# Kernel optimization log

Hardware: AMD Instinct MI355X
Metric: run time of the kernel (lower is better)

## Reference

```python
import jax, jax.numpy as jnp
import numpy as np

N_NODES = 100000
N_EDGES = 600000
D_FEAT = 128


def setup_inputs() -> dict:
    key = jax.random.key(0)
    kx, kh, kt, kp = jax.random.split(key, 4)
    x = jax.random.normal(kx, (N_NODES, D_FEAT), dtype=jnp.float32)
    # ensure every node appears at least once as a source (h) so deg > 0
    base = jax.random.permutation(kp, jnp.arange(N_NODES, dtype=jnp.int64))
    extra = jax.random.randint(kh, (N_EDGES - N_NODES,), 0, N_NODES, dtype=jnp.int64)
    h = jnp.concatenate([base, extra])
    t = jax.random.randint(kt, (N_EDGES,), 0, N_NODES, dtype=jnp.int64)
    return {"x": x, "h": h, "t": t}


def reference(x, h, t):
    n = x.shape[0]
    # degree of source nodes h  (torch_geometric.utils.degree)
    deg = jnp.zeros((n,), dtype=x.dtype).at[h].add(jnp.asarray(1, x.dtype))
    deg_inv_sqrt = deg ** -0.5
    norm = deg_inv_sqrt[t] * deg_inv_sqrt[h]  # [E]
    # spmm with row=t, col=h: out[t] += norm * x[h]
    msgs = norm[:, None] * x[h]  # [E, D]
    out = jax.ops.segment_sum(msgs, t, num_segments=n)  # [N, D]
    return jax.nn.relu(out)
```

## Files before the change

kernel.cpp:

```cpp
#include <hip/hip_runtime.h>

#define D_FEAT 128
#define KB 16
#define CBINS 25600
#define CNR 4
#define NWIN 25
#define PBINS 12800
#define PNR 8
#define CBLK 1024
#define SCAN_BLK 1024

__device__ __forceinline__ unsigned short f2bf_rtn(float f) {
    unsigned int u = __float_as_uint(f);
    unsigned int r = (u + 0x7FFFu + ((u >> 16) & 1u)) >> 16;
    return (unsigned short)r;
}

__global__ void __launch_bounds__(CBLK) count_convert_kernel(
    const int* __restrict__ h, const int* __restrict__ t,
    unsigned* __restrict__ tmat, unsigned* __restrict__ hmat,
    int* __restrict__ wsums,
    const float* __restrict__ x, unsigned short* __restrict__ xb,
    int E, int slice4, int n4)
{
    __shared__ unsigned cnt[CBINS / 2];
    const int nt = CNR * KB;
    int bid = blockIdx.x;
    if (bid >= 2 * nt) {
        int idx = (bid - 2 * nt) * CBLK + threadIdx.x;
        if (idx < n4) {
            float4 v = reinterpret_cast<const float4*>(x)[idx];
            ushort4 o;
            o.x = f2bf_rtn(v.x); o.y = f2bf_rtn(v.y);
            o.z = f2bf_rtn(v.z); o.w = f2bf_rtn(v.w);
            reinterpret_cast<ushort4*>(xb)[idx] = o;
        }
        return;
    }
    bool isT = bid < nt;
    int id2 = isT ? bid : bid - nt;
    int team = id2 / KB;
    int b = id2 - team * KB;
    int base = team * CBINS;
    for (int i = threadIdx.x; i < CBINS / 2; i += CBLK) cnt[i] = 0;
    __syncthreads();
    const int* key = isT ? t : h;
    int lo = b * slice4;
    int hi = min(lo + slice4, E);
    if (lo < hi) {
        int n4e = (hi - lo) >> 2;
        const int4* key4 = reinterpret_cast<const int4*>(key + lo);
        for (int i = threadIdx.x; i < n4e; i += CBLK) {
            int4 k = key4[i];
            unsigned d;
            d = (unsigned)(k.x - base); if (d < CBINS) atomicAdd(&cnt[d >> 1], 1u << ((d & 1) << 4));
            d = (unsigned)(k.y - base); if (d < CBINS) atomicAdd(&cnt[d >> 1], 1u << ((d & 1) << 4));
            d = (unsigned)(k.z - base); if (d < CBINS) atomicAdd(&cnt[d >> 1], 1u << ((d & 1) << 4));
            d = (unsigned)(k.w - base); if (d < CBINS) atomicAdd(&cnt[d >> 1], 1u << ((d & 1) << 4));
        }
        for (int i = lo + (n4e << 2) + threadIdx.x; i < hi; i += CBLK) {
            unsigned d = (unsigned)(key[i] - base);
            if (d < CBINS) atomicAdd(&cnt[d >> 1], 1u << ((d & 1) << 4));
        }
    }
    __syncthreads();
    unsigned* dst = (isT ? tmat : hmat) + (size_t)id2 * (CBINS / 2);
    for (int i = threadIdx.x; i < CBINS / 2; i += CBLK) dst[i] = cnt[i];
    if (isT) {
        int tid = threadIdx.x;
        if (tid < NWIN * 32) {
            int wdw = tid >> 5, l = tid & 31;
            unsigned s = 0;
            int b0 = wdw * 512 + l * 16;
            #pragma unroll
            for (int k2 = 0; k2 < 16; ++k2) {
                unsigned v = cnt[b0 + k2];
                s += (v & 0xFFFFu) + (v >> 16);
            }
            s += __shfl_down(s, 16, 32);
            s += __shfl_down(s, 8, 32);
            s += __shfl_down(s, 4, 32);
            s += __shfl_down(s, 2, 32);
            s += __shfl_down(s, 1, 32);
            if (l == 0) wsums[id2 * NWIN + wdw] = (int)s;
        }
    }
}

__global__ void __launch_bounds__(SCAN_BLK) scanfin_kernel(
    const unsigned short* __restrict__ tmat16, const unsigned short* __restrict__ hmat16,
    const int* __restrict__ wsums,
    int* __restrict__ row_ptr, int* __restrict__ cur, float* __restrict__ dis,
    int n, int E)
{
    int c = blockIdx.x;
    int tid = threadIdx.x;
    int node = c * SCAN_BLK + tid;
    int lane = tid & 63;
    int wv = tid >> 6;

    int p = 0;
    int tot = c * KB;
    for (int idx = tid; idx < tot; idx += SCAN_BLK) {
        int c2 = idx >> 4;
        int b = idx & (KB - 1);
        int team = c2 / NWIN;
        int wdw = c2 - team * NWIN;
        p += wsums[(team * KB + b) * NWIN + wdw];
    }
    #pragma unroll
    for (int off = 32; off > 0; off >>= 1) p += __shfl_down(p, off, 64);
    __shared__ int red[16];
    if (lane == 0) red[wv] = p;
    __syncthreads();
    __shared__ int prefix;
    if (tid == 0) {
        int s = 0;
        #pragma unroll
        for (int k = 0; k < 16; ++k) s += red[k];
        prefix = s;
    }

    int cnts[KB];
    int v = 0, deg = 0;
    if (node < n) {
        int cteam = node / CBINS;
        int cbin = node - cteam * CBINS;
        #pragma unroll
        for (int b = 0; b < KB; ++b) {
            size_t rowo = (size_t)(cteam * KB + b) * CBINS + cbin;
            int cv = tmat16[rowo];
            cnts[b] = cv;
            v += cv;
            deg += hmat16[rowo];
        }
    } else {
        #pragma unroll
        for (int b = 0; b < KB; ++b) cnts[b] = 0;
    }

    int s = v;
    #pragma unroll
    for (int off = 1; off < 64; off <<= 1) {
        int u = __shfl_up(s, off, 64);
        if (lane >= off) s += u;
    }
    __shared__ int wsum2[16];
    if (lane == 63) wsum2[wv] = s;
    __syncthreads();
    if (tid < 16) {
        int ws2 = wsum2[tid];
        #pragma unroll
        for (int off = 1; off < 16; off <<= 1) {
            int u = __shfl_up(ws2, off, 16);
            if ((tid & 15) >= off) ws2 += u;
        }
        wsum2[tid] = ws2;
    }
    __syncthreads();
    int basew = (wv > 0) ? wsum2[wv - 1] : 0;
    int excl = basew + s - v;

    if (node < n) {
        int run = prefix + excl;
        row_ptr[node] = run;
        int pteam = node / PBINS;
        int pbin = node - pteam * PBINS;
        #pragma unroll
        for (int b = 0; b < KB; ++b) {
            cur[(size_t)(pteam * KB + b) * PBINS + pbin] = run;
            run += cnts[b];
        }
        dis[node] = rsqrtf((float)deg);
        if (node == n - 1) row_ptr[n] = E;
    }
}

__global__ void __launch_bounds__(CBLK) place_kernel(
    const int* __restrict__ h, const int* __restrict__ t,
    const int* __restrict__ cur, int* __restrict__ edge_src,
    int E, int slice4)
{
    __shared__ int c[PBINS];
    int id2 = blockIdx.x;
    int team = id2 / KB;
    int b = id2 - team * KB;
    int base = team * PBINS;
    const int* src = cur + (size_t)id2 * PBINS;
    for (int i = threadIdx.x; i < PBINS; i += CBLK) c[i] = src[i];
    __syncthreads();
    int lo = b * slice4;
    int hi = min(lo + slice4, E);
    if (lo >= hi) return;
    int n4 = (hi - lo) >> 2;
    const int4* t4 = reinterpret_cast<const int4*>(t + lo);
    const int4* h4 = reinterpret_cast<const int4*>(h + lo);
    for (int i = threadIdx.x; i < n4; i += CBLK) {
        int4 tt = t4[i];
        int4 hh = h4[i];
        unsigned d;
        d = (unsigned)(tt.x - base); if (d < PBINS) edge_src[atomicAdd(&c[d], 1)] = hh.x;
        d = (unsigned)(tt.y - base); if (d < PBINS) edge_src[atomicAdd(&c[d], 1)] = hh.y;
        d = (unsigned)(tt.z - base); if (d < PBINS) edge_src[atomicAdd(&c[d], 1)] = hh.z;
        d = (unsigned)(tt.w - base); if (d < PBINS) edge_src[atomicAdd(&c[d], 1)] = hh.w;
    }
    for (int i = lo + (n4 << 2) + threadIdx.x; i < hi; i += CBLK) {
        unsigned d = (unsigned)(t[i] - base);
        if (d < PBINS) edge_src[atomicAdd(&c[d], 1)] = h[i];
    }
}

__global__ void gather_bf16_kernel(const unsigned int* __restrict__ xb,
                                   const int* __restrict__ row_ptr,
                                   const int* __restrict__ edge_src,
                                   const float* __restrict__ dis,
                                   float* __restrict__ out, int n) {
    int gid = blockIdx.x * blockDim.x + threadIdx.x;
    int node = gid >> 4;
    int j = gid & 15;
    if (node >= n) return;
    int beg = row_ptr[node];
    int end = row_ptr[node + 1];
    const uint4* x16 = reinterpret_cast<const uint4*>(xb);
    float a0 = 0.f, a1 = 0.f, a2 = 0.f, a3 = 0.f, a4 = 0.f, a5 = 0.f, a6 = 0.f, a7 = 0.f;
    for (int k = beg; k < end; k += 4) {
        #pragma unroll
        for (int u = 0; u < 4; ++u) {
            int kk = k + u;
            bool m = kk < end;
            int idx = m ? kk : (end - 1);
            int s = edge_src[idx];
            float nr = m ? dis[s] : 0.f;
            uint4 v = x16[(size_t)s * 16 + j];
            a0 = fmaf(nr, __uint_as_float(v.x << 16), a0);
            a1 = fmaf(nr, __uint_as_float(v.x & 0xFFFF0000u), a1);
            a2 = fmaf(nr, __uint_as_float(v.y << 16), a2);
            a3 = fmaf(nr, __uint_as_float(v.y & 0xFFFF0000u), a3);
            a4 = fmaf(nr, __uint_as_float(v.z << 16), a4);
            a5 = fmaf(nr, __uint_as_float(v.z & 0xFFFF0000u), a5);
            a6 = fmaf(nr, __uint_as_float(v.w << 16), a6);
            a7 = fmaf(nr, __uint_as_float(v.w & 0xFFFF0000u), a7);
        }
    }
    float dd = dis[node];
    float4 r0, r1;
    r0.x = fmaxf(dd * a0, 0.f); r0.y = fmaxf(dd * a1, 0.f);
    r0.z = fmaxf(dd * a2, 0.f); r0.w = fmaxf(dd * a3, 0.f);
    r1.x = fmaxf(dd * a4, 0.f); r1.y = fmaxf(dd * a5, 0.f);
    r1.z = fmaxf(dd * a6, 0.f); r1.w = fmaxf(dd * a7, 0.f);
    float4* o4 = reinterpret_cast<float4*>(out) + (size_t)node * 32 + j * 2;
    o4[0] = r0;
    o4[1] = r1;
}

__global__ void gather_f32_kernel(const float* __restrict__ x, const int* __restrict__ row_ptr,
                                  const int* __restrict__ edge_src, const float* __restrict__ dis,
                                  float* __restrict__ out, int n) {
    int gid = blockIdx.x * blockDim.x + threadIdx.x;
    int node = gid >> 5;
    int j = gid & 31;
    if (node >= n) return;
    int beg = row_ptr[node];
    int end = row_ptr[node + 1];
    const float4* x4 = reinterpret_cast<const float4*>(x);
    float4 acc = make_float4(0.f, 0.f, 0.f, 0.f);
    for (int k = beg; k < end; k += 4) {
        #pragma unroll
        for (int u = 0; u < 4; ++u) {
            int kk = k + u;
            bool m = kk < end;
            int idx = m ? kk : (end - 1);
            int s = edge_src[idx];
            float nr = m ? dis[s] : 0.f;
            float4 vv = x4[(size_t)s * 32 + j];
            acc.x = fmaf(nr, vv.x, acc.x);
            acc.y = fmaf(nr, vv.y, acc.y);
            acc.z = fmaf(nr, vv.z, acc.z);
            acc.w = fmaf(nr, vv.w, acc.w);
        }
    }
    float dd = dis[node];
    float4 r;
    r.x = fmaxf(dd * acc.x, 0.f);
    r.y = fmaxf(dd * acc.y, 0.f);
    r.z = fmaxf(dd * acc.z, 0.f);
    r.w = fmaxf(dd * acc.w, 0.f);
    reinterpret_cast<float4*>(out)[(size_t)node * 32 + j] = r;
}

extern "C" void kernel_launch(void* const* d_in, const int* in_sizes, int n_in,
                              void* d_out, int out_size, void* d_ws, size_t ws_size,
                              hipStream_t stream) {
    const float* x = (const float*)d_in[0];
    const int*   h = (const int*)d_in[1];
    const int*   t = (const int*)d_in[2];
    float* out = (float*)d_out;

    int N = in_sizes[0] / D_FEAT;
    int E = in_sizes[1];
    int nb = (N + SCAN_BLK - 1) / SCAN_BLK;

    char* w = (char*)d_ws;
    size_t off = 0;
    auto alloc = [&](size_t bytes) {
        char* p = w + off;
        off = (off + bytes + 255) & ~(size_t)255;
        return p;
    };
    unsigned* tmat    = (unsigned*)alloc((size_t)CNR * KB * (CBINS / 2) * 4);
    unsigned* hmat    = (unsigned*)alloc((size_t)CNR * KB * (CBINS / 2) * 4);
    int*      wsums   = (int*)alloc((size_t)CNR * KB * NWIN * 4);
    int*      row_ptr = (int*)alloc((size_t)(N + 1) * 4);
    int*      cur     = (int*)alloc((size_t)PNR * KB * PBINS * 4);
    float*    dis     = (float*)alloc((size_t)N * 4);
    int*      edge_src= (int*)alloc((size_t)E * 4);
    size_t core = off;
    unsigned short* xb = (unsigned short*)alloc((size_t)N * D_FEAT * 2);
    bool use_bf16 = (off <= ws_size);
    if (!use_bf16 && core > ws_size) return;

    int slice4 = (((E + KB - 1) / KB) + 3) & ~3;
    int n4 = use_bf16 ? (N * D_FEAT) / 4 : 0;
    int conv_blocks = (n4 + CBLK - 1) / CBLK;

    count_convert_kernel<<<2 * CNR * KB + conv_blocks, CBLK, 0, stream>>>(
        h, t, tmat, hmat, wsums, x, xb, E, slice4, n4);

    scanfin_kernel<<<nb, SCAN_BLK, 0, stream>>>(
        (const unsigned short*)tmat, (const unsigned short*)hmat, wsums,
        row_ptr, cur, dis, N, E);

    place_kernel<<<PNR * KB, CBLK, 0, stream>>>(h, t, cur, edge_src, E, slice4);

    if (use_bf16) {
        long long gt = (long long)N * 16;
        gather_bf16_kernel<<<(int)((gt + 255) / 256), 256, 0, stream>>>(
            (const unsigned int*)xb, row_ptr, edge_src, dis, out, N);
    } else {
        long long gt = (long long)N * 32;
        gather_f32_kernel<<<(int)((gt + 255) / 256), 256, 0, stream>>>(
            x, row_ptr, edge_src, dis, out, N);
    }
}
```

Baseline: 73.06 us.

## Prescale bf16 features by inverse sqrt degree and drop per-edge norm loads

```diff
diff --git a/kernel.cpp b/kernel.cpp
--- a/kernel.cpp
+++ b/kernel.cpp
@@ -16,27 +16,36 @@
     return (unsigned short)r;
 }
 
-__global__ void __launch_bounds__(CBLK) count_convert_kernel(
+__device__ __forceinline__ void convert_chunk_scaled(const float* __restrict__ x,
+                                                     const float* __restrict__ dis,
+                                                     unsigned short* __restrict__ xb,
+                                                     int idx, int N) {
+    int row = idx >> 5;
+    if (row > N) return;
+    int c = idx & 31;
+    size_t o = (size_t)row * 32 + c;
+    ushort4 ov;
+    if (row < N) {
+        float4 v = reinterpret_cast<const float4*>(x)[o];
+        float sc = dis[row];
+        ov.x = f2bf_rtn(v.x * sc);
+        ov.y = f2bf_rtn(v.y * sc);
+        ov.z = f2bf_rtn(v.z * sc);
+        ov.w = f2bf_rtn(v.w * sc);
+    } else {
+        ov.x = ov.y = ov.z = ov.w = 0;
+    }
+    reinterpret_cast<ushort4*>(xb)[o] = ov;
+}
+
+__global__ void __launch_bounds__(CBLK) count_kernel(
     const int* __restrict__ h, const int* __restrict__ t,
     unsigned* __restrict__ tmat, unsigned* __restrict__ hmat,
-    int* __restrict__ wsums,
-    const float* __restrict__ x, unsigned short* __restrict__ xb,
-    int E, int slice4, int n4)
+    int* __restrict__ wsums, int E, int slice4)
 {
     __shared__ unsigned cnt[CBINS / 2];
     const int nt = CNR * KB;
     int bid = blockIdx.x;
-    if (bid >= 2 * nt) {
-        int idx = (bid - 2 * nt) * CBLK + threadIdx.x;
-        if (idx < n4) {
-            float4 v = reinterpret_cast<const float4*>(x)[idx];
-            ushort4 o;
-            o.x = f2bf_rtn(v.x); o.y = f2bf_rtn(v.y);
-            o.z = f2bf_rtn(v.z); o.w = f2bf_rtn(v.w);
-            reinterpret_cast<ushort4*>(xb)[idx] = o;
-        }
-        return;
-    }
     bool isT = bid < nt;
     int id2 = isT ? bid : bid - nt;
     int team = id2 / KB;
@@ -176,11 +185,19 @@
     }
 }
 
-__global__ void __launch_bounds__(CBLK) place_kernel(
+__global__ void __launch_bounds__(CBLK) place_conv_kernel(
     const int* __restrict__ h, const int* __restrict__ t,
     const int* __restrict__ cur, int* __restrict__ edge_src,
-    int E, int slice4)
+    int E, int slice4,
+    const float* __restrict__ x, const float* __restrict__ dis,
+    unsigned short* __restrict__ xb, int N)
 {
+    const int np = PNR * KB;
+    if ((int)blockIdx.x >= np) {
+        int idx = (blockIdx.x - np) * CBLK + threadIdx.x;
+        convert_chunk_scaled(x, dis, xb, idx, N);
+        return;
+    }
     __shared__ int c[PBINS];
     int id2 = blockIdx.x;
     int team = id2 / KB;
@@ -227,19 +244,16 @@
         #pragma unroll
         for (int u = 0; u < 4; ++u) {
             int kk = k + u;
-            bool m = kk < end;
-            int idx = m ? kk : (end - 1);
-            int s = edge_src[idx];
-            float nr = m ? dis[s] : 0.f;
+            int s = (kk < end) ? edge_src[kk] : n;
             uint4 v = x16[(size_t)s * 16 + j];
-            a0 = fmaf(nr, __uint_as_float(v.x << 16), a0);
-            a1 = fmaf(nr, __uint_as_float(v.x & 0xFFFF0000u), a1);
-            a2 = fmaf(nr, __uint_as_float(v.y << 16), a2);
-            a3 = fmaf(nr, __uint_as_float(v.y & 0xFFFF0000u), a3);
-            a4 = fmaf(nr, __uint_as_float(v.z << 16), a4);
-            a5 = fmaf(nr, __uint_as_float(v.z & 0xFFFF0000u), a5);
-            a6 = fmaf(nr, __uint_as_float(v.w << 16), a6);
-            a7 = fmaf(nr, __uint_as_float(v.w & 0xFFFF0000u), a7);
+            a0 += __uint_as_float(v.x << 16);
+            a1 += __uint_as_float(v.x & 0xFFFF0000u);
+            a2 += __uint_as_float(v.y << 16);
+            a3 += __uint_as_float(v.y & 0xFFFF0000u);
+            a4 += __uint_as_float(v.z << 16);
+            a5 += __uint_as_float(v.z & 0xFFFF0000u);
+            a6 += __uint_as_float(v.w << 16);
+            a7 += __uint_as_float(v.w & 0xFFFF0000u);
         }
     }
     float dd = dis[node];
@@ -315,22 +329,22 @@
     float*    dis     = (float*)alloc((size_t)N * 4);
     int*      edge_src= (int*)alloc((size_t)E * 4);
     size_t core = off;
-    unsigned short* xb = (unsigned short*)alloc((size_t)N * D_FEAT * 2);
+    unsigned short* xb = (unsigned short*)alloc((size_t)(N + 1) * D_FEAT * 2);
     bool use_bf16 = (off <= ws_size);
     if (!use_bf16 && core > ws_size) return;
 
     int slice4 = (((E + KB - 1) / KB) + 3) & ~3;
-    int n4 = use_bf16 ? (N * D_FEAT) / 4 : 0;
-    int conv_blocks = (n4 + CBLK - 1) / CBLK;
-
-    count_convert_kernel<<<2 * CNR * KB + conv_blocks, CBLK, 0, stream>>>(
-        h, t, tmat, hmat, wsums, x, xb, E, slice4, n4);
+    int conv_n = use_bf16 ? (N + 1) * 32 : 0;
+    int conv_blocks = (conv_n + CBLK - 1) / CBLK;
+
+    count_kernel<<<2 * CNR * KB, CBLK, 0, stream>>>(h, t, tmat, hmat, wsums, E, slice4);
 
     scanfin_kernel<<<nb, SCAN_BLK, 0, stream>>>(
         (const unsigned short*)tmat, (const unsigned short*)hmat, wsums,
         row_ptr, cur, dis, N, E);
 
-    place_kernel<<<PNR * KB, CBLK, 0, stream>>>(h, t, cur, edge_src, E, slice4);
+    place_conv_kernel<<<PNR * KB + conv_blocks, CBLK, 0, stream>>>(
+        h, t, cur, edge_src, E, slice4, x, dis, xb, N);
 
     if (use_bf16) {
         long long gt = (long long)N * 16;
```

Result: slower. 75.81 us (+3.8%).
